# Performance work log

Measured on AMD Instinct MI355X. Metric: run time of the kernel, lower is better.

The kernel has to match this reference:

```python
import jax, jax.numpy as jnp
import numpy as np

N0, N1, N2 = 200_000, 100_000, 80_000
F = 32
K5, K3 = 125, 27
M1, M2, M3, M4 = 20_000, 20_000, 30_000, 20_000
EPS = 1e-5


def sparse_conv(feats, W, in_idx, out_idx, n_out):
    """Gather-GEMM-scatter sparse conv. feats:[Nin,Cin], W:[K,Cin,Cout],
    in_idx/out_idx:[K,M] kernel map. Returns [n_out, Cout]."""
    g = feats[in_idx]                                  # [K, M, Cin] gather
    contrib = jnp.einsum('kmc,kcd->kmd', g, W)         # per-offset GEMM
    cout = W.shape[-1]
    out = jnp.zeros((n_out, cout), feats.dtype)
    return out.at[out_idx.reshape(-1)].add(contrib.reshape(-1, cout))


def bn(x, g, b):
    m = x.mean(0)
    v = x.var(0)
    return (x - m) * jax.lax.rsqrt(v + EPS) * g + b


def setup_inputs():
    key = jax.random.key(0)
    ks = jax.random.split(key, 16)
    W_SCALE = 0.02
    inp = {
        'x_feats': jax.random.normal(ks[0], (N0, 1), jnp.float32),
        'w1a': jax.random.normal(ks[1], (K5, 1, F), jnp.float32) * W_SCALE,
        'w1b': jax.random.normal(ks[2], (K5, F, F), jnp.float32) * W_SCALE,
        'w1c': jax.random.normal(ks[3], (K5, F, F), jnp.float32) * W_SCALE,
        'w2': jax.random.normal(ks[4], (K3, F, 2 * F), jnp.float32) * W_SCALE,
        'w3a': jax.random.normal(ks[5], (K3, 2 * F, 4 * F), jnp.float32) * W_SCALE,
        'w3b': jax.random.normal(ks[6], (K3, 4 * F, 8 * F), jnp.float32) * W_SCALE,
        'bn1b_g': jnp.ones((F,), jnp.float32), 'bn1b_b': jnp.zeros((F,), jnp.float32),
        'bn1c_g': jnp.ones((F,), jnp.float32), 'bn1c_b': jnp.zeros((F,), jnp.float32),
        'bn3a_g': jnp.ones((4 * F,), jnp.float32), 'bn3a_b': jnp.zeros((4 * F,), jnp.float32),
        'bn3b_g': jnp.ones((8 * F,), jnp.float32), 'bn3b_b': jnp.zeros((8 * F,), jnp.float32),
        'km1a_in': jax.random.randint(ks[7], (K5, M1), 0, N0, jnp.int32),
        'km1a_out': jax.random.randint(ks[8], (K5, M1), 0, N1, jnp.int32),
        'km1b_in': jax.random.randint(ks[9], (K5, M2), 0, N1, jnp.int32),
        'km1b_out': jax.random.randint(ks[10], (K5, M2), 0, N1, jnp.int32),
        'km1c_in': jax.random.randint(ks[11], (K5, M2), 0, N1, jnp.int32),
        'km1c_out': jax.random.randint(ks[12], (K5, M2), 0, N1, jnp.int32),
        'km2_in': jax.random.randint(ks[13], (K3, M3), 0, N1, jnp.int32),
        'km2_out': jax.random.randint(ks[14], (K3, M3), 0, N2, jnp.int32),
        'km3a_in': jax.random.randint(jax.random.fold_in(key, 20), (K3, M4), 0, N2, jnp.int32),
        'km3a_out': jax.random.randint(jax.random.fold_in(key, 21), (K3, M4), 0, N2, jnp.int32),
        'km3b_in': jax.random.randint(jax.random.fold_in(key, 22), (K3, M4), 0, N2, jnp.int32),
        'km3b_out': jax.random.randint(jax.random.fold_in(key, 23), (K3, M4), 0, N2, jnp.int32),
        'n1': N1,
        'n2': N2,
    }
    return inp


def reference(x_feats, w1a, w1b, w1c, w2, w3a, w3b,
              bn1b_g, bn1b_b, bn1c_g, bn1c_b, bn3a_g, bn3a_b, bn3b_g, bn3b_b,
              km1a_in, km1a_out, km1b_in, km1b_out, km1c_in, km1c_out,
              km2_in, km2_out, km3a_in, km3a_out, km3b_in, km3b_out, n1, n2):
    # enc1: conv(1->F, k5, s2) + ReLU
    h = jax.nn.relu(sparse_conv(x_feats, w1a, km1a_in, km1a_out, n1))
    # conv(F->F, k5) + BN + ReLU
    h = jax.nn.relu(bn(sparse_conv(h, w1b, km1b_in, km1b_out, n1), bn1b_g, bn1b_b))
    # conv(F->F, k5) + BN + ReLU
    x_e1 = jax.nn.relu(bn(sparse_conv(h, w1c, km1c_in, km1c_out, n1), bn1c_g, bn1c_b))
    # conv2: conv(F->2F, k3) onto c_out coordinates (no activation)
    h2 = sparse_conv(x_e1, w2, km2_in, km2_out, n2)
    # enc2: conv(2F->4F, k3) + BN + ReLU
    h2 = jax.nn.relu(bn(sparse_conv(h2, w3a, km3a_in, km3a_out, n2), bn3a_g, bn3a_b))
    # conv(4F->8F, k3) + BN + ReLU
    x_e2 = jax.nn.relu(bn(sparse_conv(h2, w3b, km3b_in, km3b_out, n2), bn3b_g, bn3b_b))
    return (x_e1, x_e2)
```

## Files before the change

### kernel.cpp

```cpp
#include <hip/hip_runtime.h>
#include <hip/hip_fp16.h>
#include <cstdint>
#include <algorithm>

#define N1c 100000
#define N2c 80000
#define EPSc 1e-5f
#define STRIDE_N1 102400
#define STRIDE_N2 81920

typedef _Float16 fp16x8 __attribute__((ext_vector_type(8)));
typedef float f32x4 __attribute__((ext_vector_type(4)));

__global__ __launch_bounds__(256) void rank2d_kernel(
    const int* __restrict__ out_idx, int* __restrict__ rank,
    int* __restrict__ bins, int E, int M, int q, int stride)
{
    for (int e = blockIdx.x * 256 + threadIdx.x; e < E; e += gridDim.x * 256) {
        int chunk = (e / M) / q;
        rank[e] = atomicAdd(&bins[chunk * stride + out_idx[e]], 1);
    }
}

__global__ __launch_bounds__(256) void scan1(
    const int* __restrict__ bins, int* __restrict__ ptr,
    int* __restrict__ bsums, int n)
{
    __shared__ int lds[256];
    int base = blockIdx.x * 1024;
    int v[4]; int t = 0;
    #pragma unroll
    for (int i = 0; i < 4; ++i) {
        int idx = base + threadIdx.x * 4 + i;
        v[i] = idx < n ? bins[idx] : 0;
        t += v[i];
    }
    lds[threadIdx.x] = t; __syncthreads();
    for (int off = 1; off < 256; off <<= 1) {
        int x = threadIdx.x >= off ? lds[threadIdx.x - off] : 0;
        __syncthreads();
        lds[threadIdx.x] += x;
        __syncthreads();
    }
    int run = lds[threadIdx.x] - t;
    if (threadIdx.x == 255) bsums[blockIdx.x] = lds[255];
    #pragma unroll
    for (int i = 0; i < 4; ++i) {
        int idx = base + threadIdx.x * 4 + i;
        if (idx < n) ptr[idx] = run;
        run += v[i];
    }
}

__global__ __launch_bounds__(64) void scan2s(
    int* __restrict__ bsums, int bpc, int nch)
{
    int c = threadIdx.x;
    if (c < nch) {
        int run = 0;
        for (int i = 0; i < bpc; ++i) {
            int idx = c * bpc + i;
            int t = bsums[idx]; bsums[idx] = run; run += t;
        }
    }
}

__global__ __launch_bounds__(256) void scan3(
    int* __restrict__ ptr, const int* __restrict__ bsums, int n)
{
    int idx = blockIdx.x * 1024 + threadIdx.x * 4;
    int add = bsums[blockIdx.x];
    #pragma unroll
    for (int i = 0; i < 4; ++i)
        if (idx + i < n) ptr[idx + i] += add;
}

__global__ __launch_bounds__(256) void wconv_fp16(
    const float* __restrict__ W, _Float16* __restrict__ Wh,
    int K, int CIN, int CTILE, int WST, int total)
{
    for (int idx = blockIdx.x * 256 + threadIdx.x; idx < total;
         idx += gridDim.x * 256) {
        int k = idx / (CTILE * CIN);
        int c = (idx / CIN) % CTILE;
        int j = idx % CIN;
        Wh[idx] = (_Float16)W[(size_t)k * CIN * WST + (size_t)j * WST + c];
    }
}

__global__ __launch_bounds__(256) void scatter_1a(
    const float* __restrict__ x, const int* __restrict__ iin,
    const int* __restrict__ iout, const int* __restrict__ ptr,
    const int* __restrict__ rank, float2* __restrict__ payload, int E, int M)
{
    for (int e = blockIdx.x * 256 + threadIdx.x; e < E; e += gridDim.x * 256) {
        int k = e / M;
        float2 p; p.x = x[iin[e]]; p.y = __int_as_float(k);
        payload[ptr[iout[e]] + rank[e]] = p;
    }
}

__global__ __launch_bounds__(256) void phaseB_1a(
    const float2* __restrict__ payload, const int* __restrict__ ptr,
    const float* __restrict__ W, __half* __restrict__ out, int n)
{
    __shared__ float Wl[125 * 32];
    for (int i = threadIdx.x; i < 125 * 32; i += 256) Wl[i] = W[i];
    __syncthreads();
    int total = n * 32;
    for (int idx = blockIdx.x * 256 + threadIdx.x; idx < total; idx += gridDim.x * 256) {
        int o = idx >> 5, c = idx & 31;
        int s0 = ptr[o], s1 = ptr[o + 1];
        float acc = 0.f;
        for (int s = s0; s < s1; ++s) {
            float2 p = payload[s];
            acc = fmaf(p.x, Wl[(__float_as_int(p.y) << 5) + c], acc);
        }
        out[idx] = __float2half(fmaxf(acc, 0.f));
    }
}

template <int CIN, int CTILE, int GMODE, int IN16>
__global__ __launch_bounds__(256, 3) void phaseA_mfma(
    const void* __restrict__ feats_, const _Float16* __restrict__ Wh,
    const int* __restrict__ in_idx, const int* __restrict__ out_idx,
    const int* __restrict__ ptr, const int* __restrict__ rank,
    __half* __restrict__ contrib, int M,
    const float* __restrict__ sc, const float* __restrict__ sh)
{
    constexpr int PP  = 64;
    constexpr int NK  = CIN / 32;
    constexpr int NCF = CTILE / 16;
    constexpr int GCHK = CIN / 8;
    constexpr int GSM  = (GCHK < 16 ? GCHK : 16) - 1;
    constexpr int RCH  = GCHK / 4;
    static_assert(CIN % 32 == 0 && CTILE % 16 == 0 && RCH >= 1, "");

    __shared__ __align__(16) _Float16 Gl[PP * CIN];
    __shared__ __align__(16) _Float16 Wt[CTILE * CIN];
    __shared__ int sslot[PP];

    const int tid  = threadIdx.x;
    const int wave = tid >> 6;
    const int lane = tid & 63;
    const int k    = blockIdx.y;

    const int* iin  = in_idx  + (size_t)k * M;
    const int* iout = out_idx + (size_t)k * M;
    const int* rk   = rank    + (size_t)k * M;
    const _Float16* Wk = Wh + (size_t)k * CTILE * CIN;

    for (int i = tid; i < CTILE * GCHK; i += 256) {
        int row = i / GCHK, ch = i % GCHK;
        fp16x8 v = *(const fp16x8*)&Wk[(size_t)row * CIN + ch * 8];
        *(fp16x8*)&Wt[row * CIN + ((ch ^ (row & GSM)) << 3)] = v;
    }

    for (int base = blockIdx.x * PP; base < M; base += gridDim.x * PP) {
        if (tid < PP && base + tid < M)
            sslot[tid] = ptr[iout[base + tid]] + rk[base + tid];

        {
            int r = tid & 63;
            int h = tid >> 6;
            int p = base + r;
            if (p < M) {
                const int c0 = h * (CIN / 4);
                if (IN16) {
                    const _Float16* fr =
                        (const _Float16*)feats_ + (size_t)iin[p] * CIN + c0;
                    #pragma unroll
                    for (int cc = 0; cc < RCH; ++cc) {
                        int c = cc * 8;
                        fp16x8 v = *(const fp16x8*)(fr + c);
                        if (GMODE == 2) {
                            #pragma unroll
                            for (int j = 0; j < 8; ++j) {
                                float x = fmaf((float)v[j], sc[c0 + c + j],
                                               sh[c0 + c + j]);
                                v[j] = (_Float16)fmaxf(x, 0.f);
                            }
                        }
                        int ch = (c0 + c) >> 3;
                        *(fp16x8*)&Gl[r * CIN + ((ch ^ (r & GSM)) << 3)] = v;
                    }
                } else {
                    const float* fr =
                        (const float*)feats_ + (size_t)iin[p] * CIN + c0;
                    #pragma unroll
                    for (int cc = 0; cc < RCH; ++cc) {
                        int c = cc * 8;
                        float a[8];
                        *(float4*)&a[0] = *(const float4*)(fr + c);
                        *(float4*)&a[4] = *(const float4*)(fr + c + 4);
                        if (GMODE == 2) {
                            #pragma unroll
                            for (int j = 0; j < 8; ++j)
                                a[j] = fmaxf(fmaf(a[j], sc[c0 + c + j],
                                                  sh[c0 + c + j]), 0.f);
                        }
                        fp16x8 v;
                        #pragma unroll
                        for (int j = 0; j < 8; ++j) v[j] = (_Float16)a[j];
                        int ch = (c0 + c) >> 3;
                        *(fp16x8*)&Gl[r * CIN + ((ch ^ (r & GSM)) << 3)] = v;
                    }
                }
            }
        }
        __syncthreads();

        f32x4 acc[NCF];
        #pragma unroll
        for (int cf = 0; cf < NCF; ++cf)
            acc[cf] = (f32x4){0.f, 0.f, 0.f, 0.f};

        const int lrow = lane & 15;
        const int lk8  = (lane >> 4) * 8;
        #pragma unroll
        for (int kk = 0; kk < NK; ++kk) {
            int col = kk * 32 + lk8;
            int r = wave * 16 + lrow;
            fp16x8 afr = *(const fp16x8*)
                &Gl[r * CIN + ((((col >> 3) ^ (r & GSM))) << 3)];
            #pragma unroll
            for (int cf = 0; cf < NCF; ++cf) {
                int rw = cf * 16 + lrow;
                fp16x8 bfr = *(const fp16x8*)
                    &Wt[rw * CIN + ((((col >> 3) ^ (rw & GSM))) << 3)];
                acc[cf] = __builtin_amdgcn_mfma_f32_16x16x32_f16(
                    afr, bfr, acc[cf], 0, 0, 0);
            }
        }

        {
            int prb = wave * 16 + (lane >> 4) * 4;
            #pragma unroll
            for (int b = 0; b < 4; ++b) {
                int pr = prb + b;
                if (base + pr < M) {
                    size_t s = (size_t)sslot[pr];
                    #pragma unroll
                    for (int cf = 0; cf < NCF; ++cf)
                        contrib[s * CTILE + cf * 16 + lrow] =
                            __float2half(acc[cf][b]);
                }
            }
        }
        __syncthreads();
    }
}

template <int GMODE>
__global__ __launch_bounds__(256, 3) void phaseA_mfma_3b(
    const void* __restrict__ feats_, const _Float16* __restrict__ Wh,
    const int* __restrict__ in_idx, const int* __restrict__ out_idx,
    const int* __restrict__ ptr, const int* __restrict__ rank,
    __half* __restrict__ contrib, int M,
    const float* __restrict__ sc, const float* __restrict__ sh)
{
    constexpr int CIN = 128, PP = 64, NK = 4, NCF = 8;
    constexpr int GCHK = 16, GSM = 15, RCH = 4;

    __shared__ __align__(16) _Float16 Gl[PP * CIN];
    __shared__ __align__(16) _Float16 Wt[128 * CIN];
    __shared__ int sslot[PP];

    const int tid  = threadIdx.x;
    const int wave = tid >> 6;
    const int lane = tid & 63;
    const int k    = blockIdx.y;

    const _Float16* feats = (const _Float16*)feats_;
    const int* iin  = in_idx  + (size_t)k * M;
    const int* iout = out_idx + (size_t)k * M;
    const int* rk   = rank    + (size_t)k * M;
    const _Float16* Wk = Wh + (size_t)k * 256 * CIN;

    const int lrow = lane & 15;
    const int lk8  = (lane >> 4) * 8;

    for (int base = blockIdx.x * PP; base < M; base += gridDim.x * PP) {
        if (tid < PP && base + tid < M)
            sslot[tid] = ptr[iout[base + tid]] + rk[base + tid];

        {
            int r = tid & 63;
            int h = tid >> 6;
            int p = base + r;
            if (p < M) {
                const int c0 = h * 32;
                const _Float16* fr = feats + (size_t)iin[p] * CIN + c0;
                #pragma unroll
                for (int cc = 0; cc < RCH; ++cc) {
                    int c = cc * 8;
                    fp16x8 v = *(const fp16x8*)(fr + c);
                    if (GMODE == 2) {
                        #pragma unroll
                        for (int j = 0; j < 8; ++j) {
                            float x = fmaf((float)v[j], sc[c0 + c + j],
                                           sh[c0 + c + j]);
                            v[j] = (_Float16)fmaxf(x, 0.f);
                        }
                    }
                    int ch = (c0 + c) >> 3;
                    *(fp16x8*)&Gl[r * CIN + ((ch ^ (r & GSM)) << 3)] = v;
                }
            }
        }

        #pragma unroll
        for (int half = 0; half < 2; ++half) {
            __syncthreads();
            for (int i = tid; i < 128 * GCHK; i += 256) {
                int row = i / GCHK, ch = i % GCHK;
                fp16x8 v = *(const fp16x8*)
                    &Wk[(size_t)(half * 128 + row) * CIN + ch * 8];
                *(fp16x8*)&Wt[row * CIN + ((ch ^ (row & GSM)) << 3)] = v;
            }
            __syncthreads();

            f32x4 acc[NCF];
            #pragma unroll
            for (int cf = 0; cf < NCF; ++cf)
                acc[cf] = (f32x4){0.f, 0.f, 0.f, 0.f};

            #pragma unroll
            for (int kk = 0; kk < NK; ++kk) {
                int col = kk * 32 + lk8;
                int r = wave * 16 + lrow;
                fp16x8 afr = *(const fp16x8*)
                    &Gl[r * CIN + ((((col >> 3) ^ (r & GSM))) << 3)];
                #pragma unroll
                for (int cf = 0; cf < NCF; ++cf) {
                    int rw = cf * 16 + lrow;
                    fp16x8 bfr = *(const fp16x8*)
                        &Wt[rw * CIN + ((((col >> 3) ^ (rw & GSM))) << 3)];
                    acc[cf] = __builtin_amdgcn_mfma_f32_16x16x32_f16(
                        afr, bfr, acc[cf], 0, 0, 0);
                }
            }

            int prb = wave * 16 + (lane >> 4) * 4;
            #pragma unroll
            for (int b = 0; b < 4; ++b) {
                int pr = prb + b;
                if (base + pr < M) {
                    size_t s = (size_t)sslot[pr];
                    #pragma unroll
                    for (int cf = 0; cf < NCF; ++cf)
                        contrib[s * 256 + half * 128 + cf * 16 + lrow] =
                            __float2half(acc[cf][b]);
                }
            }
        }
        __syncthreads();
    }
}

template <int CSTR, bool STATS, int OUT16>
__global__ __launch_bounds__(256) void phaseB8(
    const __half* __restrict__ contrib, const int* __restrict__ ptr,
    void* __restrict__ out_, int n, int ostr, int accum,
    double* __restrict__ statsbuf, int sqoff)
{
    float s1 = 0.f, s2 = 0.f;
    int total = n * CSTR;
    for (int idx = blockIdx.x * 256 + threadIdx.x; idx < total; idx += gridDim.x * 256) {
        int o = idx / CSTR, c = idx % CSTR;
        int a = ptr[o], b = ptr[o + 1];
        size_t oi = (size_t)o * ostr + c;
        float acc;
        if (OUT16)
            acc = accum ? __half2float(((const __half*)out_)[oi]) : 0.f;
        else
            acc = accum ? ((const float*)out_)[oi] : 0.f;
        for (int s = a; s < b; ++s)
            acc += __half2float(contrib[(size_t)s * CSTR + c]);
        if (OUT16) ((__half*)out_)[oi] = __float2half(acc);
        else       ((float*)out_)[oi] = acc;
        if (STATS) { s1 += acc; s2 += acc * acc; }
    }
    if constexpr (STATS) {
        __shared__ double l1[256], l2[256];
        l1[threadIdx.x] = (double)s1; l2[threadIdx.x] = (double)s2;
        __syncthreads();
        for (int off = 128; off >= CSTR; off >>= 1) {
            if (threadIdx.x < (unsigned)off) {
                l1[threadIdx.x] += l1[threadIdx.x + off];
                l2[threadIdx.x] += l2[threadIdx.x + off];
            }
            __syncthreads();
        }
        if (threadIdx.x < CSTR) {
            atomicAdd(&statsbuf[threadIdx.x], l1[threadIdx.x]);
            atomicAdd(&statsbuf[sqoff + threadIdx.x], l2[threadIdx.x]);
        }
    }
}

template <int C>
__global__ __launch_bounds__(256) void make_scsh(
    const double* __restrict__ sums, const float* __restrict__ g,
    const float* __restrict__ b, float* __restrict__ sc, float* __restrict__ sh,
    double inv_n)
{
    int c = threadIdx.x;
    if (c < C) {
        double mean = sums[c] * inv_n;
        double var  = sums[C + c] * inv_n - mean * mean;
        float s = g[c] * (float)(1.0 / sqrt(var + (double)EPSc));
        sc[c] = s;
        sh[c] = b[c] - (float)mean * s;
    }
}

template <int C>
__global__ __launch_bounds__(256) void bn_apply_relu_kernel(
    float* __restrict__ x, int n, const double* __restrict__ sums,
    const float* __restrict__ g, const float* __restrict__ b)
{
    const int c = threadIdx.x % C;
    const double inv_n = 1.0 / (double)n;
    double mean = sums[c] * inv_n;
    double var  = sums[C + c] * inv_n - mean * mean;
    float scale = g[c] * (float)(1.0 / sqrt(var + (double)EPSc));
    float shift = b[c] - (float)mean * scale;
    size_t total = (size_t)n * C;
    size_t stride = (size_t)gridDim.x * 256;
    for (size_t i = (size_t)blockIdx.x * 256 + threadIdx.x; i < total; i += stride)
        x[i] = fmaxf(x[i] * scale + shift, 0.f);
}

template <int C>
__global__ __launch_bounds__(256) void bn_apply_relu_shadow_kernel(
    float* __restrict__ x, __half* __restrict__ xh, int n,
    const double* __restrict__ sums,
    const float* __restrict__ g, const float* __restrict__ b)
{
    const int c = threadIdx.x % C;
    const double inv_n = 1.0 / (double)n;
    double mean = sums[c] * inv_n;
    double var  = sums[C + c] * inv_n - mean * mean;
    float scale = g[c] * (float)(1.0 / sqrt(var + (double)EPSc));
    float shift = b[c] - (float)mean * scale;
    size_t total = (size_t)n * C;
    size_t stride = (size_t)gridDim.x * 256;
    for (size_t i = (size_t)blockIdx.x * 256 + threadIdx.x; i < total; i += stride) {
        float v = fmaxf(x[i] * scale + shift, 0.f);
        x[i] = v;
        xh[i] = __float2half(v);
    }
}

struct Plan { int q, nch; };

static Plan make_plan(long long tot_elems, int K, long long cap, int maxch)
{
    if (cap < 1) cap = 1;
    long long nch0 = (tot_elems + cap - 1) / cap;
    if (nch0 < 1) nch0 = 1;
    if (nch0 > K) nch0 = K;
    int q = (int)((K + nch0 - 1) / nch0);
    int nch = (K + q - 1) / q;
    if (nch > maxch) { q = (K + maxch - 1) / maxch; nch = (K + q - 1) / q; }
    return { q, nch };
}

static void build_csr2d(const int* iout, int* rank, int* bins, int* ptr, int* bsums,
                        int E, int M, int q, int nch, int stride, hipStream_t s)
{
    hipMemsetAsync(bins, 0, (size_t)nch * stride * sizeof(int), s);
    int gb = std::min(2048, (E + 255) / 256);
    hipLaunchKernelGGL(rank2d_kernel, dim3(gb), dim3(256), 0, s, iout, rank, bins, E, M, q, stride);
    int totalbins = nch * stride, nb = totalbins / 1024, bpc = stride / 1024;
    hipLaunchKernelGGL(scan1, dim3(nb), dim3(256), 0, s, bins, ptr, bsums, totalbins);
    hipLaunchKernelGGL(scan2s, dim3(1), dim3(64), 0, s, bsums, bpc, nch);
    hipLaunchKernelGGL(scan3, dim3(nb), dim3(256), 0, s, ptr, bsums, totalbins);
}

template <int CIN, int COUT, int GMODE, bool STATS, int IN16, int OUT16>
static void run_layer(const void* feats, const float* W,
                      const int* iin, const int* iout, void* outp,
                      int M, int K, int n_out, int stride, int maxch,
                      int* bins, int* ptr, int* bsums, int* rank, __half* contrib,
                      _Float16* wh, long long cap_f32,
                      const float* sc, const float* sh,
                      double* statsbuf, hipStream_t s)
{
    int wtot = K * COUT * CIN;
    hipLaunchKernelGGL(wconv_fp16, dim3(std::min(2048, (wtot + 255) / 256)),
                       dim3(256), 0, s, W, wh, K, CIN, COUT, COUT, wtot);
    long long cap_h = cap_f32 * 2;
    Plan pl = make_plan((long long)K * M * COUT, K, cap_h, maxch);
    build_csr2d(iout, rank, bins, ptr, bsums, K * M, M, pl.q, pl.nch, stride, s);
    for (int ch = 0; ch < pl.nch; ++ch) {
        int k0 = ch * pl.q;
        int qc = std::min(pl.q, K - k0);
        dim3 g((M + 63) / 64, qc);
        hipLaunchKernelGGL((phaseA_mfma<CIN, COUT, GMODE, IN16>), g, dim3(256), 0, s,
                           feats, wh + (size_t)k0 * COUT * CIN,
                           iin + (size_t)k0 * M, iout + (size_t)k0 * M,
                           ptr + (size_t)ch * stride, rank + (size_t)k0 * M,
                           contrib, M, sc, sh);
        bool last = (ch == pl.nch - 1);
        if (STATS && last)
            hipLaunchKernelGGL((phaseB8<COUT, true, OUT16>), dim3(2048), dim3(256), 0, s,
                               contrib, ptr + (size_t)ch * stride, outp, n_out, COUT,
                               ch ? 1 : 0, statsbuf, COUT);
        else
            hipLaunchKernelGGL((phaseB8<COUT, false, OUT16>), dim3(2048), dim3(256), 0, s,
                               contrib, ptr + (size_t)ch * stride, outp, n_out, COUT,
                               ch ? 1 : 0, (double*)nullptr, 0);
    }
}

extern "C" void kernel_launch(void* const* d_in, const int* in_sizes, int n_in,
                              void* d_out, int out_size, void* d_ws, size_t ws_size,
                              hipStream_t stream)
{
    const float* x_feats = (const float*)d_in[0];
    const float* w1a = (const float*)d_in[1];
    const float* w1b = (const float*)d_in[2];
    const float* w1c = (const float*)d_in[3];
    const float* w2  = (const float*)d_in[4];
    const float* w3a = (const float*)d_in[5];
    const float* w3b = (const float*)d_in[6];
    const float* bn1b_g = (const float*)d_in[7];
    const float* bn1b_b = (const float*)d_in[8];
    const float* bn1c_g = (const float*)d_in[9];
    const float* bn1c_b = (const float*)d_in[10];
    const float* bn3a_g = (const float*)d_in[11];
    const float* bn3a_b = (const float*)d_in[12];
    const float* bn3b_g = (const float*)d_in[13];
    const float* bn3b_b = (const float*)d_in[14];
    const int* km1a_in  = (const int*)d_in[15];
    const int* km1a_out = (const int*)d_in[16];
    const int* km1b_in  = (const int*)d_in[17];
    const int* km1b_out = (const int*)d_in[18];
    const int* km1c_in  = (const int*)d_in[19];
    const int* km1c_out = (const int*)d_in[20];
    const int* km2_in   = (const int*)d_in[21];
    const int* km2_out  = (const int*)d_in[22];
    const int* km3a_in  = (const int*)d_in[23];
    const int* km3a_out = (const int*)d_in[24];
    const int* km3b_in  = (const int*)d_in[25];
    const int* km3b_out = (const int*)d_in[26];

    float* out  = (float*)d_out;
    float* x_e1 = out;
    float* x_e2 = out + (size_t)N1c * 32;

    float* ws = (float*)d_ws;
    float*  poolA  = ws;
    float*  poolB  = poolA + 10240000;
    double* dstats = (double*)(poolB + 5120000);
    float*  scsh   = (float*)(dstats + 2048);
    int*    bins   = (int*)(scsh + 1024);
    int*    ptr    = bins + 819200;
    int*    bsums  = ptr + 819200;
    int*    rank   = bsums + 1024;
    float*  whf    = (float*)(rank + 2500000);
    _Float16* wh   = (_Float16*)whf;
    float*  contribf = whf + 442400;
    __half* contrib  = (__half*)contribf;
    const long long FIXED = 10240000LL + 5120000 + 4096 + 1024
                          + 819200 + 819200 + 1024 + 2500000 + 442400;
    long long cap = (long long)(ws_size / 4) - FIXED - 32;
    if (cap < 1) cap = 1;

    __half* h1  = (__half*)poolA;
    __half* h3  = (__half*)poolA;
    __half* h2  = (__half*)poolB;
    __half* h2b = (__half*)poolB;
    __half* xe1h = (__half*)poolB + 5120000;

    double* dst1b = dstats;
    double* dst1c = dstats + 512;
    double* dst3a = dstats + 1024;
    double* dst3b = dstats + 1536;
    float* sc1b = scsh,       *sh1b = scsh + 32;
    float* sc3a = scsh + 256, *sh3a = scsh + 384;

    hipMemsetAsync(dstats, 0, 2048 * sizeof(double), stream);

    {
        build_csr2d(km1a_out, rank, bins, ptr, bsums, 125 * 20000, 20000, 125, 1,
                    STRIDE_N1, stream);
        hipLaunchKernelGGL(scatter_1a, dim3(2048), dim3(256), 0, stream,
                           x_feats, km1a_in, km1a_out, ptr, rank, (float2*)contribf,
                           125 * 20000, 20000);
        hipLaunchKernelGGL(phaseB_1a, dim3(2048), dim3(256), 0, stream,
                           (const float2*)contribf, ptr, w1a, h1, N1c);
    }

    run_layer<32, 32, 0, true, 1, 1>(h1, w1b, km1b_in, km1b_out, h2, 20000, 125, N1c,
                                     STRIDE_N1, 8, bins, ptr, bsums, rank, contrib,
                                     wh, cap, nullptr, nullptr, dst1b, stream);
    hipLaunchKernelGGL((make_scsh<32>), dim3(1), dim3(256), 0, stream,
                       dst1b, bn1b_g, bn1b_b, sc1b, sh1b, 1.0 / N1c);

    run_layer<32, 32, 2, true, 1, 0>(h2, w1c, km1c_in, km1c_out, x_e1, 20000, 125, N1c,
                                     STRIDE_N1, 8, bins, ptr, bsums, rank, contrib,
                                     wh, cap, sc1b, sh1b, dst1c, stream);
    hipLaunchKernelGGL((bn_apply_relu_shadow_kernel<32>), dim3(2048), dim3(256), 0, stream,
                       x_e1, xe1h, N1c, dst1c, bn1c_g, bn1c_b);

    run_layer<32, 64, 0, false, 1, 1>(xe1h, w2, km2_in, km2_out, h2b, 30000, 27, N2c,
                                      STRIDE_N2, 10, bins, ptr, bsums, rank, contrib,
                                      wh, cap, nullptr, nullptr, nullptr, stream);

    run_layer<64, 128, 0, true, 1, 1>(h2b, w3a, km3a_in, km3a_out, h3, 20000, 27, N2c,
                                      STRIDE_N2, 10, bins, ptr, bsums, rank, contrib,
                                      wh, cap, nullptr, nullptr, dst3a, stream);
    hipLaunchKernelGGL((make_scsh<128>), dim3(1), dim3(256), 0, stream,
                       dst3a, bn3a_g, bn3a_b, sc3a, sh3a, 1.0 / N2c);

    {
        const int M = 20000, K = 27;
        int wtot = K * 256 * 128;
        hipLaunchKernelGGL(wconv_fp16, dim3(2048), dim3(256), 0, stream,
                           w3b, wh, K, 128, 256, 256, wtot);
        Plan pl = make_plan((long long)K * M * 256, K, cap * 2, 10);
        build_csr2d(km3b_out, rank, bins, ptr, bsums, K * M, M, pl.q, pl.nch,
                    STRIDE_N2, stream);
        for (int ch = 0; ch < pl.nch; ++ch) {
            int k0 = ch * pl.q;
            int qc = std::min(pl.q, K - k0);
            dim3 g((M + 63) / 64, qc);
            hipLaunchKernelGGL((phaseA_mfma_3b<2>), g, dim3(256), 0, stream,
                               (const void*)h3, wh + (size_t)k0 * 256 * 128,
                               km3b_in + (size_t)k0 * M, km3b_out + (size_t)k0 * M,
                               ptr + (size_t)ch * STRIDE_N2, rank + (size_t)k0 * M,
                               contrib, M, sc3a, sh3a);
            bool last = (ch == pl.nch - 1);
            if (last)
                hipLaunchKernelGGL((phaseB8<256, true, 0>), dim3(2048), dim3(256), 0, stream,
                                   contrib, ptr + (size_t)ch * STRIDE_N2,
                                   x_e2, N2c, 256, ch ? 1 : 0, dst3b, 256);
            else
                hipLaunchKernelGGL((phaseB8<256, false, 0>), dim3(2048), dim3(256), 0, stream,
                                   contrib, ptr + (size_t)ch * STRIDE_N2,
                                   x_e2, N2c, 256, ch ? 1 : 0, (double*)nullptr, 0);
        }
        hipLaunchKernelGGL((bn_apply_relu_kernel<256>), dim3(2048), dim3(256), 0, stream,
                           x_e2, N2c, dst3b, bn3b_g, bn3b_b);
    }
}
```

Measured before the change: 1.841 ms.

## Vectorize phaseB8 reduction and keep 3b chunk partials in fp16 scratch

phaseB8 now has each thread handle four channels, using half2 loads of contrib, packed fp16 or float4 stores, and per-lane stat accumulators reduced in shared memory. For the 3b layer, intermediate chunk partial sums go to an fp16 scratch buffer, and only the last chunk reads it and writes the fp32 output. This cuts per-element index math, widens memory transactions, and halves the traffic for partial accumulations. In exchange, partial sums are rounded to fp16 between chunks, and the scratch buffer must fit in poolA.

```diff
diff --git a/kernel.cpp b/kernel.cpp
--- a/kernel.cpp
+++ b/kernel.cpp
@@ -358,43 +358,97 @@
     }
 }
 
-template <int CSTR, bool STATS, int OUT16>
+template <int CSTR, bool STATS, int OUT16, int PARTIN>
 __global__ __launch_bounds__(256) void phaseB8(
     const __half* __restrict__ contrib, const int* __restrict__ ptr,
-    void* __restrict__ out_, int n, int ostr, int accum,
+    void* __restrict__ out_, const __half* __restrict__ part_in,
+    int n, int ostr, int accum,
     double* __restrict__ statsbuf, int sqoff)
 {
-    float s1 = 0.f, s2 = 0.f;
-    int total = n * CSTR;
-    for (int idx = blockIdx.x * 256 + threadIdx.x; idx < total; idx += gridDim.x * 256) {
-        int o = idx / CSTR, c = idx % CSTR;
+    constexpr int V = 4;
+    constexpr int TPR = CSTR / V;
+    static_assert(CSTR % 4 == 0 && 256 % TPR == 0, "");
+    float s1[V] = {0.f, 0.f, 0.f, 0.f}, s2[V] = {0.f, 0.f, 0.f, 0.f};
+    int total = n * TPR;
+    for (int idx = blockIdx.x * 256 + threadIdx.x; idx < total;
+         idx += gridDim.x * 256) {
+        int o  = idx / TPR;
+        int c0 = (idx % TPR) * V;
         int a = ptr[o], b = ptr[o + 1];
-        size_t oi = (size_t)o * ostr + c;
-        float acc;
-        if (OUT16)
-            acc = accum ? __half2float(((const __half*)out_)[oi]) : 0.f;
-        else
-            acc = accum ? ((const float*)out_)[oi] : 0.f;
-        for (int s = a; s < b; ++s)
-            acc += __half2float(contrib[(size_t)s * CSTR + c]);
-        if (OUT16) ((__half*)out_)[oi] = __float2half(acc);
-        else       ((float*)out_)[oi] = acc;
-        if (STATS) { s1 += acc; s2 += acc * acc; }
+        size_t obase = (size_t)o * ostr + c0;
+        float acc[V];
+        if (accum) {
+            if (PARTIN) {
+                const __half2* pp =
+                    (const __half2*)(part_in + (size_t)o * CSTR + c0);
+                __half2 p0 = pp[0], p1 = pp[1];
+                acc[0] = __low2float(p0); acc[1] = __high2float(p0);
+                acc[2] = __low2float(p1); acc[3] = __high2float(p1);
+            } else if (OUT16) {
+                const __half2* pp = (const __half2*)((const __half*)out_ + obase);
+                __half2 p0 = pp[0], p1 = pp[1];
+                acc[0] = __low2float(p0); acc[1] = __high2float(p0);
+                acc[2] = __low2float(p1); acc[3] = __high2float(p1);
+            } else {
+                float4 f = *(const float4*)((const float*)out_ + obase);
+                acc[0] = f.x; acc[1] = f.y; acc[2] = f.z; acc[3] = f.w;
+            }
+        } else {
+            #pragma unroll
+            for (int j = 0; j < V; ++j) acc[j] = 0.f;
+        }
+        for (int s = a; s < b; ++s) {
+            const __half2* cp =
+                (const __half2*)(contrib + (size_t)s * CSTR + c0);
+            __half2 q0 = cp[0], q1 = cp[1];
+            acc[0] += __low2float(q0); acc[1] += __high2float(q0);
+            acc[2] += __low2float(q1); acc[3] += __high2float(q1);
+        }
+        if (OUT16) {
+            __half2 h0 = __floats2half2_rn(acc[0], acc[1]);
+            __half2 h1 = __floats2half2_rn(acc[2], acc[3]);
+            uint2 pk;
+            pk.x = *(unsigned int*)&h0;
+            pk.y = *(unsigned int*)&h1;
+            *(uint2*)((__half*)out_ + obase) = pk;
+        } else {
+            float4 f;
+            f.x = acc[0]; f.y = acc[1]; f.z = acc[2]; f.w = acc[3];
+            *(float4*)((float*)out_ + obase) = f;
+        }
+        if (STATS) {
+            #pragma unroll
+            for (int j = 0; j < V; ++j) {
+                s1[j] += acc[j];
+                s2[j] += acc[j] * acc[j];
+            }
+        }
     }
     if constexpr (STATS) {
-        __shared__ double l1[256], l2[256];
-        l1[threadIdx.x] = (double)s1; l2[threadIdx.x] = (double)s2;
+        __shared__ double l1[256][V], l2[256][V];
+        #pragma unroll
+        for (int j = 0; j < V; ++j) {
+            l1[threadIdx.x][j] = (double)s1[j];
+            l2[threadIdx.x][j] = (double)s2[j];
+        }
         __syncthreads();
-        for (int off = 128; off >= CSTR; off >>= 1) {
+        for (int off = 128; off >= TPR; off >>= 1) {
             if (threadIdx.x < (unsigned)off) {
-                l1[threadIdx.x] += l1[threadIdx.x + off];
-                l2[threadIdx.x] += l2[threadIdx.x + off];
+                #pragma unroll
+                for (int j = 0; j < V; ++j) {
+                    l1[threadIdx.x][j] += l1[threadIdx.x + off][j];
+                    l2[threadIdx.x][j] += l2[threadIdx.x + off][j];
+                }
             }
             __syncthreads();
         }
-        if (threadIdx.x < CSTR) {
-            atomicAdd(&statsbuf[threadIdx.x], l1[threadIdx.x]);
-            atomicAdd(&statsbuf[sqoff + threadIdx.x], l2[threadIdx.x]);
+        if (threadIdx.x < TPR) {
+            #pragma unroll
+            for (int j = 0; j < V; ++j) {
+                atomicAdd(&statsbuf[threadIdx.x * V + j], l1[threadIdx.x][j]);
+                atomicAdd(&statsbuf[sqoff + threadIdx.x * V + j],
+                          l2[threadIdx.x][j]);
+            }
         }
     }
 }
@@ -505,12 +559,14 @@
                            contrib, M, sc, sh);
         bool last = (ch == pl.nch - 1);
         if (STATS && last)
-            hipLaunchKernelGGL((phaseB8<COUT, true, OUT16>), dim3(2048), dim3(256), 0, s,
-                               contrib, ptr + (size_t)ch * stride, outp, n_out, COUT,
+            hipLaunchKernelGGL((phaseB8<COUT, true, OUT16, 0>), dim3(2048), dim3(256), 0, s,
+                               contrib, ptr + (size_t)ch * stride, outp,
+                               (const __half*)nullptr, n_out, COUT,
                                ch ? 1 : 0, statsbuf, COUT);
         else
-            hipLaunchKernelGGL((phaseB8<COUT, false, OUT16>), dim3(2048), dim3(256), 0, s,
-                               contrib, ptr + (size_t)ch * stride, outp, n_out, COUT,
+            hipLaunchKernelGGL((phaseB8<COUT, false, OUT16, 0>), dim3(2048), dim3(256), 0, s,
+                               contrib, ptr + (size_t)ch * stride, outp,
+                               (const __half*)nullptr, n_out, COUT,
                                ch ? 1 : 0, (double*)nullptr, 0);
     }
 }
@@ -574,6 +630,7 @@
     __half* h2  = (__half*)poolB;
     __half* h2b = (__half*)poolB;
     __half* xe1h = (__half*)poolB + 5120000;
+    __half* xpart = (__half*)(poolA + 5120000);
 
     double* dst1b = dstats;
     double* dst1c = dstats + 512;
@@ -634,14 +691,21 @@
                                ptr + (size_t)ch * STRIDE_N2, rank + (size_t)k0 * M,
                                contrib, M, sc3a, sh3a);
             bool last = (ch == pl.nch - 1);
-            if (last)
-                hipLaunchKernelGGL((phaseB8<256, true, 0>), dim3(2048), dim3(256), 0, stream,
+            if (!last)
+                hipLaunchKernelGGL((phaseB8<256, false, 1, 0>), dim3(2048), dim3(256), 0, stream,
                                    contrib, ptr + (size_t)ch * STRIDE_N2,
-                                   x_e2, N2c, 256, ch ? 1 : 0, dst3b, 256);
+                                   xpart, (const __half*)nullptr, N2c, 256,
+                                   ch ? 1 : 0, (double*)nullptr, 0);
+            else if (ch == 0)
+                hipLaunchKernelGGL((phaseB8<256, true, 0, 0>), dim3(2048), dim3(256), 0, stream,
+                                   contrib, ptr + (size_t)ch * STRIDE_N2,
+                                   x_e2, (const __half*)nullptr, N2c, 256,
+                                   0, dst3b, 256);
             else
-                hipLaunchKernelGGL((phaseB8<256, false, 0>), dim3(2048), dim3(256), 0, stream,
+                hipLaunchKernelGGL((phaseB8<256, true, 0, 1>), dim3(2048), dim3(256), 0, stream,
                                    contrib, ptr + (size_t)ch * STRIDE_N2,
-                                   x_e2, N2c, 256, ch ? 1 : 0, (double*)nullptr, 0);
+                                   x_e2, xpart, N2c, 256,
+                                   1, dst3b, 256);
         }
         hipLaunchKernelGGL((bn_apply_relu_kernel<256>), dim3(2048), dim3(256), 0, stream,
                            x_e2, N2c, dst3b, bn3b_g, bn3b_b);
```

After: 2.177 ms. 1.18x slower.
